# Kernel tuning notes

Measured on AMD Instinct MI355X. Metric: run time of the kernel, lower is better.

The kernel has to match this reference:

```python
import jax, jax.numpy as jnp
import numpy as np
from jax import lax

BIT = 9
QMAX = float(2 ** (BIT - 1) - 1)  # 255 for 9-bit symmetric


def fake_quant(v):
    """Symmetric per-tensor 9-bit fake quantization with STE."""
    scale = jnp.max(jnp.abs(v)) / QMAX
    scale = jnp.where(scale > 0, scale, jnp.ones_like(scale))
    q = jnp.round(v / scale) * scale
    return v + lax.stop_gradient(q - v)


def qconv(x, w):
    xq = fake_quant(x)
    wq = fake_quant(w)
    return lax.conv_general_dilated(
        xq, wq, window_strides=(1, 1), padding='VALID',
        dimension_numbers=('NCHW', 'OIHW', 'NCHW'))


def qfc(x, w):
    # x: [B, Fin], w: [Fout, Fin]
    return jnp.einsum('bi,oi->bo', fake_quant(x), fake_quant(w))


def maxpool2(x):
    return lax.reduce_window(x, -jnp.inf, lax.max,
                             (1, 1, 2, 2), (1, 1, 2, 2), 'VALID')


def setup_inputs() -> dict:
    key = jax.random.key(0)
    ks = jax.random.split(key, 6)
    x = jax.random.uniform(ks[0], (4096, 3, 32, 32), dtype=jnp.float32)
    def winit(k, shape):
        fan_in = int(np.prod(shape[1:]))
        return jax.random.normal(k, shape, dtype=jnp.float32) / np.sqrt(fan_in)
    w1 = winit(ks[1], (6, 3, 5, 5))
    w2 = winit(ks[2], (16, 6, 5, 5))
    w3 = winit(ks[3], (120, 16, 5, 5))
    w4 = winit(ks[4], (84, 120))
    w5 = winit(ks[5], (10, 84))
    return {'x': x, 'w1': w1, 'w2': w2, 'w3': w3, 'w4': w4, 'w5': w5}


def reference(x, w1, w2, w3, w4, w5):
    h = maxpool2(jax.nn.relu(qconv(x, w1)))        # [B,6,14,14]
    h = maxpool2(jax.nn.relu(qconv(h, w2)))        # [B,16,5,5]
    h = jax.nn.relu(qconv(h, w3))                  # [B,120,1,1]
    h = h.reshape(h.shape[0], -1)                  # [B,120]
    h = jax.nn.relu(qfc(h, w4))                    # [B,84]
    return qfc(h, w5)                              # [B,10]
```

## Files before the change

### kernel.cpp

```cpp
#include <hip/hip_runtime.h>
#include <hip/hip_bf16.h>

#define QMAX 255.0f

typedef __attribute__((ext_vector_type(8))) short short8;
typedef __attribute__((ext_vector_type(4))) float f32x4;

#define OFF_BF1   16
#define OFF_BF2   2064
#define OFF_BF3   6160
#define OFF_BF4   32784
#define OFF_BF5   38928
#define OFF_H1    40960
#define OFF_H2    5545984
#define OFF_H3    40960
#define OFF_H4    532480

#define IMG1 3080
#define IMG2 1352

__device__ __forceinline__ float get_scale(const unsigned* slots, int i) {
    float amax = __uint_as_float(slots[i]);
    float s = amax / QMAX;
    if (!(s > 0.0f)) s = 1.0f;
    return s;
}
__device__ __forceinline__ unsigned f2bf(float f) { return __float_as_uint(f) >> 16; }

__device__ __forceinline__ float block_maxN(float v, float* red, int nw) {
    #pragma unroll
    for (int off = 32; off > 0; off >>= 1) v = fmaxf(v, __shfl_xor(v, off));
    if ((threadIdx.x & 63) == 0) red[threadIdx.x >> 6] = v;
    __syncthreads();
    float m = red[0];
    for (int i = 1; i < nw; i++) m = fmaxf(m, red[i]);
    return m;
}

__global__ __launch_bounds__(64) void k_zero(unsigned* __restrict__ slots) {
    if (threadIdx.x < 16) slots[threadIdx.x] = 0u;
}

__global__ __launch_bounds__(256) void k_absmax_all(
    const float4* __restrict__ x4,
    const float* __restrict__ w1, const float* __restrict__ w2,
    const float* __restrict__ w3, const float* __restrict__ w4,
    const float* __restrict__ w5, unsigned* __restrict__ slots)
{
    __shared__ float red[4];
    int b = blockIdx.x, tid = threadIdx.x;
    float m = 0.0f;
    int slot = -1;
    if (b < 2048) {
        slot = 0;
        for (int i = b * 256 + tid; i < 3145728; i += 2048 * 256) {
            float4 v = x4[i];
            m = fmaxf(m, fmaxf(fmaxf(fabsf(v.x), fabsf(v.y)), fmaxf(fabsf(v.z), fabsf(v.w))));
        }
    } else {
        int b2 = b - 2048;
        const float* w = nullptr; int n = 0, start = 0, stride = 256;
        if (b2 < 48)      { w = w3; n = 48000; start = b2 * 256;        stride = 48 * 256; slot = 7; }
        else if (b2 < 58) { w = w4; n = 10080; start = (b2 - 48) * 256; stride = 10 * 256; slot = 8; }
        else if (b2 == 58){ w = w2; n = 2400;  slot = 6; }
        else if (b2 == 59){ w = w1; n = 450;   slot = 5; }
        else if (b2 == 60){ w = w5; n = 840;   slot = 9; }
        if (slot >= 0)
            for (int i = start + tid; i < n; i += stride) m = fmaxf(m, fabsf(w[i]));
    }
    m = block_maxN(m, red, 4);
    if (tid == 0 && slot >= 0) atomicMax(&slots[slot], __float_as_uint(m));
}

__global__ __launch_bounds__(256) void k_bfrag(
    const float* __restrict__ w1, const float* __restrict__ w2,
    const float* __restrict__ w3, const float* __restrict__ w4,
    const float* __restrict__ w5, const unsigned* __restrict__ slots,
    unsigned short* __restrict__ bf1, unsigned short* __restrict__ bf2,
    unsigned short* __restrict__ bf3, unsigned short* __restrict__ bf4,
    unsigned short* __restrict__ bf5)
{
    int idx = blockIdx.x * 256 + threadIdx.x;
    if (idx < 4096) {
        int f = idx, e = f & 7, l = (f >> 3) & 63, s = (f >> 9) & 3, H = f >> 11;
        int n = l & 15, g = l >> 4, C = 4 * s + g;
        float v = 0.f;
        if (n < 12 && C < 15) {
            int o = n >> 2, dx = n & 3, kx = e - dx;
            if (kx >= 0 && kx <= 4) {
                int c = C / 5, ky = C % 5, oc = 3 * H + o;
                v = rintf(w1[((oc * 3 + c) * 5 + ky) * 5 + kx] / get_scale(slots, 5));
            }
        }
        bf1[f] = (unsigned short)f2bf(v);
    } else if (idx < 12288) {
        int f = idx - 4096, e = f & 7, l = (f >> 3) & 63, s = (f >> 9) & 7, H = f >> 12;
        int n = l & 15, g = l >> 4, C = 4 * s + g;
        float v = 0.f;
        if (C < 30) {
            int o = n >> 1, dx = n & 1, kx = e - dx;
            if (kx >= 0 && kx <= 4) {
                int c = C / 5, ky = C % 5, oc = 8 * H + o;
                v = rintf(w2[((oc * 6 + c) * 5 + ky) * 5 + kx] / get_scale(slots, 6));
            }
        }
        bf2[f] = (unsigned short)f2bf(v);
    } else if (idx < 65536) {
        int f = idx - 12288, e = f & 7, l = (f >> 3) & 63, r = f >> 9;
        int s = r % 13, Nt = r / 13;
        int oc = Nt * 16 + (l & 15), k = 32 * s + 8 * (l >> 4) + e;
        float v = 0.f;
        if (oc < 120 && k < 400) v = rintf(w3[oc * 400 + k] / get_scale(slots, 7));
        bf3[f] = (unsigned short)f2bf(v);
    } else if (idx < 77824) {
        int f = idx - 65536, e = f & 7, l = (f >> 3) & 63, r = f >> 9;
        int s = r & 3, Nt = r >> 2;
        int oc = Nt * 16 + (l & 15), k = 32 * s + 8 * (l >> 4) + e;
        float v = 0.f;
        if (oc < 84 && k < 120) v = rintf(w4[oc * 120 + k] / get_scale(slots, 8));
        bf4[f] = (unsigned short)f2bf(v);
    } else if (idx < 79360) {
        int f = idx - 77824, e = f & 7, l = (f >> 3) & 63, s = f >> 9;
        int oc = l & 15, k = 32 * s + 8 * (l >> 4) + e;
        float v = 0.f;
        if (oc < 10 && k < 84) v = rintf(w5[oc * 84 + k] / get_scale(slots, 9));
        bf5[f] = (unsigned short)f2bf(v);
    }
}

__global__ __launch_bounds__(512) void k_conv1(
    const float* __restrict__ x, const unsigned short* __restrict__ bf1,
    const unsigned* __restrict__ slots, unsigned* __restrict__ slot_out,
    float* __restrict__ h1)
{
    __shared__ unsigned short xs[8 * IMG1];
    __shared__ float red[8];
    int b0 = blockIdx.x * 8, tid = threadIdx.x;
    int lane = tid & 63, wid = tid >> 6;
    int il = lane & 15, g = lane >> 4;
    short8 Bf[2][4];
    #pragma unroll
    for (int H = 0; H < 2; H++)
        #pragma unroll
        for (int s = 0; s < 4; s++)
            Bf[H][s] = *(const short8*)(bf1 + ((H * 4 + s) * 64 + lane) * 8);
    float sx = get_scale(slots, 0);
    #pragma unroll
    for (int img = 0; img < 8; img++) {
        const float* xb = x + (long)(b0 + img) * 3072;
        for (int i = tid; i < 1536; i += 512) {
            int c = i >> 9, rem = i & 511, yy = rem >> 4, c2 = (rem & 15) << 1;
            float2 v = *(const float2*)(xb + c * 1024 + yy * 32 + c2);
            unsigned pk = f2bf(rintf(v.x / sx)) | (f2bf(rintf(v.y / sx)) << 16);
            *(unsigned*)&xs[img * IMG1 + c * 1024 + yy * 32 + c2] = pk;
        }
    }
    __syncthreads();
    float mscale = sx * get_scale(slots, 5);

    int abase[4];
    #pragma unroll
    for (int s = 0; s < 4; s++) {
        int C = 4 * s + g; if (C > 14) C = 14;
        abase[s] = (il >> 1) * IMG1 + (C / 5) * 1024 + (C % 5) * 32;
    }
    int half = il & 1;
    int n = il, o = n >> 2, dx = n & 3;
    bool doSt = ((n & 1) == 0) && (n < 12);
    float vmax = 0.f;
    for (int uu = wid; uu < 49; uu += 8) {
        int pbe = uu / 14, pye = uu - 14 * pbe;
        int po = uu + 49;
        int pbo = po / 14, pyo = po - 14 * pbo;
        int pb = half ? pbo : pbe;
        int py = half ? pyo : pye;
        f32x4 acc[2][2];
        #pragma unroll
        for (int H = 0; H < 2; H++)
            #pragma unroll
            for (int yo = 0; yo < 2; yo++) acc[H][yo] = (f32x4){0.f, 0.f, 0.f, 0.f};
        #pragma unroll
        for (int yo = 0; yo < 2; yo++) {
            int y = 2 * py + yo;
            #pragma unroll
            for (int s = 0; s < 4; s++) {
                int addr = abase[s] + y * 32 + 4 * pb;
                union { unsigned long long u[2]; short8 v; } tA;
                tA.u[0] = *(const unsigned long long*)(xs + addr);
                tA.u[1] = *(const unsigned long long*)(xs + addr + 4);
                acc[0][yo] = __builtin_amdgcn_mfma_f32_16x16x32_bf16(tA.v, Bf[0][s], acc[0][yo], 0, 0, 0);
                acc[1][yo] = __builtin_amdgcn_mfma_f32_16x16x32_bf16(tA.v, Bf[1][s], acc[1][yo], 0, 0, 0);
            }
        }
        #pragma unroll
        for (int H = 0; H < 2; H++)
            #pragma unroll
            for (int r = 0; r < 4; r++) {
                float m = fmaxf(acc[H][0][r], acc[H][1][r]);
                float pooled = fmaxf(m, __shfl_xor(m, 1));
                if (doSt) {
                    int imgr = 2 * g + (r >> 1);
                    int pbr = (r & 1) ? pbo : pbe;
                    int pyr = (r & 1) ? pyo : pye;
                    float v = fmaxf(pooled * mscale, 0.f);
                    int oc = 3 * H + o, px = 2 * pbr + (dx >> 1);
                    h1[((long)(b0 + imgr) * 6 + oc) * 224 + pyr * 16 + px] = v;
                    vmax = fmaxf(vmax, v);
                }
            }
    }
    vmax = block_maxN(vmax, red, 8);
    if (tid == 0) atomicMax(slot_out, __float_as_uint(vmax));
}

__global__ __launch_bounds__(256) void k_conv2(
    const float* __restrict__ h1, const unsigned short* __restrict__ bf2,
    const unsigned* __restrict__ slots, unsigned* __restrict__ slot_out,
    float* __restrict__ h2)
{
    __shared__ unsigned short xs[4 * IMG2];
    __shared__ float red[4];
    int b0 = blockIdx.x * 4, tid = threadIdx.x;
    int lane = tid & 63, wid = tid >> 6;
    int il = lane & 15, g = lane >> 4;
    short8 Bf[2][8];
    #pragma unroll
    for (int H = 0; H < 2; H++)
        #pragma unroll
        for (int s = 0; s < 8; s++)
            Bf[H][s] = *(const short8*)(bf2 + ((H * 8 + s) * 64 + lane) * 8);
    float s1 = get_scale(slots, 1);
    #pragma unroll
    for (int img = 0; img < 4; img++) {
        const float4* src = (const float4*)(h1 + (long)(b0 + img) * 1344);
        for (int i = tid; i < 336; i += 256) {
            float4 v = src[i];
            unsigned pk0 = f2bf(rintf(v.x / s1)) | (f2bf(rintf(v.y / s1)) << 16);
            unsigned pk1 = f2bf(rintf(v.z / s1)) | (f2bf(rintf(v.w / s1)) << 16);
            *(uint2*)&xs[img * IMG2 + 4 * i] = make_uint2(pk0, pk1);
        }
    }
    __syncthreads();
    float mscale = s1 * get_scale(slots, 6);

    int abase[8];
    #pragma unroll
    for (int s = 0; s < 8; s++) {
        int C = 4 * s + g; if (C > 29) C = 29;
        abase[s] = (il >> 2) * IMG2 + (C / 5) * 224 + (C % 5) * 16;
    }
    int q = il & 3;
    int offq = (q == 0) ? 0 : (6 * q + 1);
    int n = il, o = n >> 1;
    bool doStCol = ((n & 1) == 0);
    float vmax = 0.f;
    for (int uu = wid; uu < 7; uu += 4) {
        int p = offq + uu; if (p > 24) p = 24;
        int pb = p / 5, py = p % 5;
        f32x4 acc[2][2];
        #pragma unroll
        for (int H = 0; H < 2; H++)
            #pragma unroll
            for (int yo = 0; yo < 2; yo++) acc[H][yo] = (f32x4){0.f, 0.f, 0.f, 0.f};
        #pragma unroll
        for (int yo = 0; yo < 2; yo++) {
            int y = 2 * py + yo;
            #pragma unroll
            for (int s = 0; s < 8; s++) {
                int addr = abase[s] + y * 16 + 2 * pb;
                union { unsigned u[4]; short8 v; } tA;
                tA.u[0] = *(const unsigned*)(xs + addr);
                tA.u[1] = *(const unsigned*)(xs + addr + 2);
                tA.u[2] = *(const unsigned*)(xs + addr + 4);
                tA.u[3] = *(const unsigned*)(xs + addr + 6);
                acc[0][yo] = __builtin_amdgcn_mfma_f32_16x16x32_bf16(tA.v, Bf[0][s], acc[0][yo], 0, 0, 0);
                acc[1][yo] = __builtin_amdgcn_mfma_f32_16x16x32_bf16(tA.v, Bf[1][s], acc[1][yo], 0, 0, 0);
            }
        }
        #pragma unroll
        for (int H = 0; H < 2; H++)
            #pragma unroll
            for (int r = 0; r < 4; r++) {
                float m = fmaxf(acc[H][0][r], acc[H][1][r]);
                float pooled = fmaxf(m, __shfl_xor(m, 1));
                int cntr = (r == 0) ? 7 : 6;
                if (doStCol && uu < cntr) {
                    int offr = (r == 0) ? 0 : (6 * r + 1);
                    int pr = offr + uu, pbr = pr / 5, pyr = pr % 5;
                    float v = fmaxf(pooled * mscale, 0.f);
                    int oc = 8 * H + o;
                    h2[((long)(b0 + g) * 16 + oc) * 25 + pyr * 5 + pbr] = v;
                    vmax = fmaxf(vmax, v);
                }
            }
    }
    vmax = block_maxN(vmax, red, 4);
    if (tid == 0) atomicMax(slot_out, __float_as_uint(vmax));
}

__global__ __launch_bounds__(512) void k_conv3(
    const float* __restrict__ h2, const unsigned short* __restrict__ bf3,
    const unsigned* __restrict__ slots, unsigned* __restrict__ slot_out,
    float* __restrict__ h3)
{
    __shared__ unsigned short xs[16 * 408];
    __shared__ float red[8];
    int b0 = blockIdx.x * 16, tid = threadIdx.x;
    int lane = tid & 63, wid = tid >> 6;
    int il = lane & 15, g = lane >> 4;
    short8 Bf[13];
    #pragma unroll
    for (int s = 0; s < 13; s++)
        Bf[s] = *(const short8*)(bf3 + ((wid * 13 + s) * 64 + lane) * 8);
    float s2 = get_scale(slots, 2);
    for (int i = tid; i < 3200; i += 512) {
        int img = i / 200, p = i % 200;
        float2 v = *(const float2*)(h2 + (long)(b0 + img) * 400 + 2 * p);
        unsigned pk = f2bf(rintf(v.x / s2)) | (f2bf(rintf(v.y / s2)) << 16);
        *(unsigned*)&xs[img * 408 + 2 * p] = pk;
    }
    __syncthreads();
    float mscale = s2 * get_scale(slots, 7);
    f32x4 acc = (f32x4){0.f, 0.f, 0.f, 0.f};
    #pragma unroll
    for (int s = 0; s < 13; s++) {
        int C = 4 * s + g; if (C > 49) C = 49;
        int addr = il * 408 + 8 * C;
        union { unsigned long long u[2]; short8 v; } tA;
        tA.u[0] = *(const unsigned long long*)(xs + addr);
        tA.u[1] = *(const unsigned long long*)(xs + addr + 4);
        acc = __builtin_amdgcn_mfma_f32_16x16x32_bf16(tA.v, Bf[s], acc, 0, 0, 0);
    }
    float vmax = 0.f;
    int oc = wid * 16 + il;
    if (oc < 120) {
        #pragma unroll
        for (int r = 0; r < 4; r++) {
            float v = fmaxf(acc[r] * mscale, 0.f);
            h3[(long)(b0 + 4 * g + r) * 120 + oc] = v;
            vmax = fmaxf(vmax, v);
        }
    }
    vmax = block_maxN(vmax, red, 8);
    if (tid == 0) atomicMax(slot_out, __float_as_uint(vmax));
}

__global__ __launch_bounds__(512) void k_fc4(
    const float* __restrict__ h3, const unsigned short* __restrict__ bf4,
    const unsigned* __restrict__ slots, unsigned* __restrict__ slot_out,
    float* __restrict__ h4)
{
    __shared__ unsigned short xs[16 * 136];
    __shared__ float red[8];
    int b0 = blockIdx.x * 16, tid = threadIdx.x;
    int lane = tid & 63, wid = tid >> 6;
    int il = lane & 15, g = lane >> 4;
    short8 Bf[4];
    if (wid < 6) {
        #pragma unroll
        for (int s = 0; s < 4; s++)
            Bf[s] = *(const short8*)(bf4 + ((wid * 4 + s) * 64 + lane) * 8);
    }
    float s3 = get_scale(slots, 3);
    for (int i = tid; i < 960; i += 512) {
        int img = i / 60, p = i % 60;
        float2 v = *(const float2*)(h3 + (long)(b0 + img) * 120 + 2 * p);
        unsigned pk = f2bf(rintf(v.x / s3)) | (f2bf(rintf(v.y / s3)) << 16);
        *(unsigned*)&xs[img * 136 + 2 * p] = pk;
    }
    __syncthreads();
    float mscale = s3 * get_scale(slots, 8);
    float vmax = 0.f;
    if (wid < 6) {
        f32x4 acc = (f32x4){0.f, 0.f, 0.f, 0.f};
        #pragma unroll
        for (int s = 0; s < 4; s++) {
            int C = 4 * s + g; if (C > 14) C = 14;
            int addr = il * 136 + 8 * C;
            union { unsigned long long u[2]; short8 v; } tA;
            tA.u[0] = *(const unsigned long long*)(xs + addr);
            tA.u[1] = *(const unsigned long long*)(xs + addr + 4);
            acc = __builtin_amdgcn_mfma_f32_16x16x32_bf16(tA.v, Bf[s], acc, 0, 0, 0);
        }
        int oc = wid * 16 + il;
        if (oc < 84) {
            #pragma unroll
            for (int r = 0; r < 4; r++) {
                float v = fmaxf(acc[r] * mscale, 0.f);
                h4[(long)(b0 + 4 * g + r) * 84 + oc] = v;
                vmax = fmaxf(vmax, v);
            }
        }
    }
    vmax = block_maxN(vmax, red, 8);
    if (tid == 0) atomicMax(slot_out, __float_as_uint(vmax));
}

__global__ __launch_bounds__(256) void k_fc5(
    const float* __restrict__ h4, const unsigned short* __restrict__ bf5,
    const unsigned* __restrict__ slots, float* __restrict__ out)
{
    __shared__ unsigned short xs[4 * 16 * 104];
    int tid = threadIdx.x;
    int lane = tid & 63, w = tid >> 6;
    int il = lane & 15, g = lane >> 4;
    int b0w = blockIdx.x * 64 + w * 16;
    short8 Bf[3];
    #pragma unroll
    for (int s = 0; s < 3; s++)
        Bf[s] = *(const short8*)(bf5 + ((s * 64) + lane) * 8);
    float s4 = get_scale(slots, 4);
    for (int i = lane; i < 672; i += 64) {
        int img = i / 42, j = i % 42;
        float2 v = *(const float2*)(h4 + (long)(b0w + img) * 84 + 2 * j);
        unsigned pk = f2bf(rintf(v.x / s4)) | (f2bf(rintf(v.y / s4)) << 16);
        *(unsigned*)&xs[w * 1664 + img * 104 + 2 * j] = pk;
    }
    for (int i = lane; i < 96; i += 64) {
        int img = i / 6, j = i % 6;
        *(unsigned*)&xs[w * 1664 + img * 104 + 84 + 2 * j] = 0u;
    }
    __syncthreads();
    float mscale = s4 * get_scale(slots, 9);
    f32x4 acc = (f32x4){0.f, 0.f, 0.f, 0.f};
    #pragma unroll
    for (int s = 0; s < 3; s++) {
        int addr = w * 1664 + il * 104 + 32 * s + 8 * g;
        union { unsigned long long u[2]; short8 v; } tA;
        tA.u[0] = *(const unsigned long long*)(xs + addr);
        tA.u[1] = *(const unsigned long long*)(xs + addr + 4);
        acc = __builtin_amdgcn_mfma_f32_16x16x32_bf16(tA.v, Bf[s], acc, 0, 0, 0);
    }
    if (il < 10) {
        #pragma unroll
        for (int r = 0; r < 4; r++)
            out[(long)(b0w + 4 * g + r) * 10 + il] = acc[r] * mscale;
    }
}

extern "C" void kernel_launch(void* const* d_in, const int* in_sizes, int n_in,
                              void* d_out, int out_size, void* d_ws, size_t ws_size,
                              hipStream_t stream) {
    const float* x  = (const float*)d_in[0];
    const float* w1 = (const float*)d_in[1];
    const float* w2 = (const float*)d_in[2];
    const float* w3 = (const float*)d_in[3];
    const float* w4 = (const float*)d_in[4];
    const float* w5 = (const float*)d_in[5];
    float* out = (float*)d_out;
    float* ws = (float*)d_ws;
    unsigned* slots = (unsigned*)d_ws;
    unsigned short* bf1 = (unsigned short*)(ws + OFF_BF1);
    unsigned short* bf2 = (unsigned short*)(ws + OFF_BF2);
    unsigned short* bf3 = (unsigned short*)(ws + OFF_BF3);
    unsigned short* bf4 = (unsigned short*)(ws + OFF_BF4);
    unsigned short* bf5 = (unsigned short*)(ws + OFF_BF5);
    float* h1 = ws + OFF_H1;
    float* h2 = ws + OFF_H2;
    float* h3 = ws + OFF_H3;
    float* h4 = ws + OFF_H4;

    k_zero<<<1, 64, 0, stream>>>(slots);
    k_absmax_all<<<2112, 256, 0, stream>>>((const float4*)x, w1, w2, w3, w4, w5, slots);
    k_bfrag<<<310, 256, 0, stream>>>(w1, w2, w3, w4, w5, slots, bf1, bf2, bf3, bf4, bf5);
    k_conv1<<<512, 512, 0, stream>>>(x, bf1, slots, slots + 1, h1);
    k_conv2<<<1024, 256, 0, stream>>>(h1, bf2, slots, slots + 2, h2);
    k_conv3<<<256, 512, 0, stream>>>(h2, bf3, slots, slots + 3, h3);
    k_fc4<<<256, 512, 0, stream>>>(h3, bf4, slots, slots + 4, h4);
    k_fc5<<<64, 256, 0, stream>>>(h4, bf5, slots, out);
}
```

Baseline: 113.8 us.

## Shrink conv1/conv2 blocks to two images and remap MFMA rows across images

Conv1 and conv2 now process two images per block instead of eight or four, launching 2048 smaller blocks each. The MFMA row mapping is rebuilt so that each 16-row tile spans eight position groups per image across two images, with per-row validity masks and start offsets. The aim is more blocks and less LDS per block, which should give better occupancy and load balance across CUs. In exchange, each block amortises its weight-fragment loads and its reduction and atomic over fewer images.

```diff
diff --git a/kernel.cpp b/kernel.cpp
--- a/kernel.cpp
+++ b/kernel.cpp
@@ -128,14 +128,14 @@
     }
 }
 
-__global__ __launch_bounds__(512) void k_conv1(
+__global__ __launch_bounds__(256) void k_conv1(
     const float* __restrict__ x, const unsigned short* __restrict__ bf1,
     const unsigned* __restrict__ slots, unsigned* __restrict__ slot_out,
     float* __restrict__ h1)
 {
-    __shared__ unsigned short xs[8 * IMG1];
-    __shared__ float red[8];
-    int b0 = blockIdx.x * 8, tid = threadIdx.x;
+    __shared__ unsigned short xs[2 * IMG1];
+    __shared__ float red[4];
+    int b0 = blockIdx.x * 2, tid = threadIdx.x;
     int lane = tid & 63, wid = tid >> 6;
     int il = lane & 15, g = lane >> 4;
     short8 Bf[2][4];
@@ -145,15 +145,13 @@
         for (int s = 0; s < 4; s++)
             Bf[H][s] = *(const short8*)(bf1 + ((H * 4 + s) * 64 + lane) * 8);
     float sx = get_scale(slots, 0);
-    #pragma unroll
-    for (int img = 0; img < 8; img++) {
-        const float* xb = x + (long)(b0 + img) * 3072;
-        for (int i = tid; i < 1536; i += 512) {
-            int c = i >> 9, rem = i & 511, yy = rem >> 4, c2 = (rem & 15) << 1;
-            float2 v = *(const float2*)(xb + c * 1024 + yy * 32 + c2);
-            unsigned pk = f2bf(rintf(v.x / sx)) | (f2bf(rintf(v.y / sx)) << 16);
-            *(unsigned*)&xs[img * IMG1 + c * 1024 + yy * 32 + c2] = pk;
-        }
+    for (int i = tid; i < 3072; i += 256) {
+        int img = (i >= 1536) ? 1 : 0;
+        int r = i - img * 1536;
+        int c = r >> 9, rem = r & 511, yy = rem >> 4, c2 = (rem & 15) << 1;
+        float2 v = *(const float2*)(x + (long)(b0 + img) * 3072 + c * 1024 + yy * 32 + c2);
+        unsigned pk = f2bf(rintf(v.x / sx)) | (f2bf(rintf(v.y / sx)) << 16);
+        *(unsigned*)&xs[img * IMG1 + c * 1024 + yy * 32 + c2] = pk;
     }
     __syncthreads();
     float mscale = sx * get_scale(slots, 5);
@@ -162,18 +160,16 @@
     #pragma unroll
     for (int s = 0; s < 4; s++) {
         int C = 4 * s + g; if (C > 14) C = 14;
-        abase[s] = (il >> 1) * IMG1 + (C / 5) * 1024 + (C % 5) * 32;
-    }
-    int half = il & 1;
+        abase[s] = (il >> 3) * IMG1 + (C / 5) * 1024 + (C % 5) * 32;
+    }
+    unsigned oct_a = il & 7;
+    unsigned start_a = 12u * oct_a + min(oct_a, 2u);
     int n = il, o = n >> 2, dx = n & 3;
     bool doSt = ((n & 1) == 0) && (n < 12);
     float vmax = 0.f;
-    for (int uu = wid; uu < 49; uu += 8) {
-        int pbe = uu / 14, pye = uu - 14 * pbe;
-        int po = uu + 49;
-        int pbo = po / 14, pyo = po - 14 * pbo;
-        int pb = half ? pbo : pbe;
-        int py = half ? pyo : pye;
+    for (unsigned uu = wid; uu < 13; uu += 4) {
+        unsigned p = start_a + uu; if (p > 97) p = 97;
+        unsigned pb = p / 14, py = p % 14;
         f32x4 acc[2][2];
         #pragma unroll
         for (int H = 0; H < 2; H++)
@@ -192,24 +188,32 @@
                 acc[1][yo] = __builtin_amdgcn_mfma_f32_16x16x32_bf16(tA.v, Bf[1][s], acc[1][yo], 0, 0, 0);
             }
         }
+        unsigned pbr[4], pyr[4]; bool val[4];
+        #pragma unroll
+        for (int r = 0; r < 4; r++) {
+            unsigned m = 4 * g + r, oct_r = m & 7;
+            unsigned cnt = 12u + (oct_r < 2 ? 1u : 0u);
+            unsigned pr = 12u * oct_r + min(oct_r, 2u) + uu;
+            val[r] = (uu < cnt);
+            pbr[r] = pr / 14; pyr[r] = pr % 14;
+        }
         #pragma unroll
         for (int H = 0; H < 2; H++)
             #pragma unroll
             for (int r = 0; r < 4; r++) {
                 float m = fmaxf(acc[H][0][r], acc[H][1][r]);
                 float pooled = fmaxf(m, __shfl_xor(m, 1));
-                if (doSt) {
-                    int imgr = 2 * g + (r >> 1);
-                    int pbr = (r & 1) ? pbo : pbe;
-                    int pyr = (r & 1) ? pyo : pye;
+                if (doSt && val[r]) {
+                    unsigned mm = 4 * g + r;
+                    int imgr = mm >> 3;
                     float v = fmaxf(pooled * mscale, 0.f);
-                    int oc = 3 * H + o, px = 2 * pbr + (dx >> 1);
-                    h1[((long)(b0 + imgr) * 6 + oc) * 224 + pyr * 16 + px] = v;
+                    int oc = 3 * H + o, px = 2 * pbr[r] + (dx >> 1);
+                    h1[((long)(b0 + imgr) * 6 + oc) * 224 + pyr[r] * 16 + px] = v;
                     vmax = fmaxf(vmax, v);
                 }
             }
     }
-    vmax = block_maxN(vmax, red, 8);
+    vmax = block_maxN(vmax, red, 4);
     if (tid == 0) atomicMax(slot_out, __float_as_uint(vmax));
 }
 
@@ -218,9 +222,9 @@
     const unsigned* __restrict__ slots, unsigned* __restrict__ slot_out,
     float* __restrict__ h2)
 {
-    __shared__ unsigned short xs[4 * IMG2];
+    __shared__ unsigned short xs[2 * IMG2];
     __shared__ float red[4];
-    int b0 = blockIdx.x * 4, tid = threadIdx.x;
+    int b0 = blockIdx.x * 2, tid = threadIdx.x;
     int lane = tid & 63, wid = tid >> 6;
     int il = lane & 15, g = lane >> 4;
     short8 Bf[2][8];
@@ -230,15 +234,13 @@
         for (int s = 0; s < 8; s++)
             Bf[H][s] = *(const short8*)(bf2 + ((H * 8 + s) * 64 + lane) * 8);
     float s1 = get_scale(slots, 1);
-    #pragma unroll
-    for (int img = 0; img < 4; img++) {
-        const float4* src = (const float4*)(h1 + (long)(b0 + img) * 1344);
-        for (int i = tid; i < 336; i += 256) {
-            float4 v = src[i];
-            unsigned pk0 = f2bf(rintf(v.x / s1)) | (f2bf(rintf(v.y / s1)) << 16);
-            unsigned pk1 = f2bf(rintf(v.z / s1)) | (f2bf(rintf(v.w / s1)) << 16);
-            *(uint2*)&xs[img * IMG2 + 4 * i] = make_uint2(pk0, pk1);
-        }
+    for (int i = tid; i < 672; i += 256) {
+        int img = (i >= 336) ? 1 : 0;
+        int r = i - img * 336;
+        float4 v = ((const float4*)(h1 + (long)(b0 + img) * 1344))[r];
+        unsigned pk0 = f2bf(rintf(v.x / s1)) | (f2bf(rintf(v.y / s1)) << 16);
+        unsigned pk1 = f2bf(rintf(v.z / s1)) | (f2bf(rintf(v.w / s1)) << 16);
+        *(uint2*)&xs[img * IMG2 + 4 * r] = make_uint2(pk0, pk1);
     }
     __syncthreads();
     float mscale = s1 * get_scale(slots, 6);
@@ -247,16 +249,17 @@
     #pragma unroll
     for (int s = 0; s < 8; s++) {
         int C = 4 * s + g; if (C > 29) C = 29;
-        abase[s] = (il >> 2) * IMG2 + (C / 5) * 224 + (C % 5) * 16;
-    }
-    int q = il & 3;
-    int offq = (q == 0) ? 0 : (6 * q + 1);
+        abase[s] = (il >> 3) * IMG2 + (C / 5) * 224 + (C % 5) * 16;
+    }
+    unsigned oct_a = il & 7;
+    unsigned start_a = 3u * oct_a + (oct_a > 0 ? 1u : 0u);
     int n = il, o = n >> 1;
     bool doStCol = ((n & 1) == 0);
     float vmax = 0.f;
-    for (int uu = wid; uu < 7; uu += 4) {
-        int p = offq + uu; if (p > 24) p = 24;
-        int pb = p / 5, py = p % 5;
+    {
+        unsigned uu = wid;
+        unsigned p = start_a + uu; if (p > 24) p = 24;
+        unsigned pb = p / 5, py = p % 5;
         f32x4 acc[2][2];
         #pragma unroll
         for (int H = 0; H < 2; H++)
@@ -277,19 +280,27 @@
                 acc[1][yo] = __builtin_amdgcn_mfma_f32_16x16x32_bf16(tA.v, Bf[1][s], acc[1][yo], 0, 0, 0);
             }
         }
+        unsigned pbr[4], pyr[4]; bool val[4];
+        #pragma unroll
+        for (int r = 0; r < 4; r++) {
+            unsigned m = 4 * g + r, oct_r = m & 7;
+            unsigned cnt = 3u + (oct_r == 0 ? 1u : 0u);
+            unsigned pr = 3u * oct_r + (oct_r > 0 ? 1u : 0u) + uu;
+            val[r] = (uu < cnt);
+            pbr[r] = pr / 5; pyr[r] = pr % 5;
+        }
         #pragma unroll
         for (int H = 0; H < 2; H++)
             #pragma unroll
             for (int r = 0; r < 4; r++) {
                 float m = fmaxf(acc[H][0][r], acc[H][1][r]);
                 float pooled = fmaxf(m, __shfl_xor(m, 1));
-                int cntr = (r == 0) ? 7 : 6;
-                if (doStCol && uu < cntr) {
-                    int offr = (r == 0) ? 0 : (6 * r + 1);
-                    int pr = offr + uu, pbr = pr / 5, pyr = pr % 5;
+                if (doStCol && val[r]) {
+                    unsigned mm = 4 * g + r;
+                    int imgr = mm >> 3;
                     float v = fmaxf(pooled * mscale, 0.f);
                     int oc = 8 * H + o;
-                    h2[((long)(b0 + g) * 16 + oc) * 25 + pyr * 5 + pbr] = v;
+                    h2[((long)(b0 + imgr) * 16 + oc) * 25 + pyr[r] * 5 + pbr[r]] = v;
                     vmax = fmaxf(vmax, v);
                 }
             }
@@ -463,8 +474,8 @@
     k_zero<<<1, 64, 0, stream>>>(slots);
     k_absmax_all<<<2112, 256, 0, stream>>>((const float4*)x, w1, w2, w3, w4, w5, slots);
     k_bfrag<<<310, 256, 0, stream>>>(w1, w2, w3, w4, w5, slots, bf1, bf2, bf3, bf4, bf5);
-    k_conv1<<<512, 512, 0, stream>>>(x, bf1, slots, slots + 1, h1);
-    k_conv2<<<1024, 256, 0, stream>>>(h1, bf2, slots, slots + 2, h2);
+    k_conv1<<<2048, 256, 0, stream>>>(x, bf1, slots, slots + 1, h1);
+    k_conv2<<<2048, 256, 0, stream>>>(h1, bf2, slots, slots + 2, h2);
     k_conv3<<<256, 512, 0, stream>>>(h2, bf3, slots, slots + 3, h3);
     k_fc4<<<256, 512, 0, stream>>>(h3, bf4, slots, slots + 4, h4);
     k_fc5<<<64, 256, 0, stream>>>(h4, bf5, slots, out);
```

Result: slower. 172.2 us (+51.3%).
